# Optimization experiments

Hardware: AMD Instinct MI355X
Metric: run time of the kernel (lower is better)

## Reference

```python
import jax, jax.numpy as jnp
import numpy as np

H = 4      # n_heads
HD = 32    # head_dim
D = 128    # pair channels = H*HD
S = 384    # sequence length
EPS = 1e-5


def setup_inputs() -> dict:
    key = jax.random.key(0)
    ks = jax.random.split(key, 8)
    return {
        "x": jax.random.normal(ks[0], (1, S, S, D), dtype=jnp.float32),
        "attn_mask": jnp.zeros((1, 1, 1, S), dtype=jnp.float32),
        "ln_w": jax.random.uniform(ks[1], (D,), dtype=jnp.float32),
        "ln_b": jax.random.normal(ks[2], (D,), dtype=jnp.float32) * 0.02,
        "bias_w": jax.random.normal(ks[3], (H, D), dtype=jnp.float32) * 0.02,
        "qkv_w": jax.random.normal(ks[4], (3 * H * HD, D), dtype=jnp.float32) * 0.02,
        "g_w": jax.random.normal(ks[5], (H * HD, D), dtype=jnp.float32) * 0.02,
        "o_w": jax.random.normal(ks[6], (D, H * HD), dtype=jnp.float32) * 0.02,
    }


def reference(x, attn_mask, ln_w, ln_b, bias_w, qkv_w, g_w, o_w):
    # x: [1, S, S, D]; ending=False -> no permute
    xs = x[0]  # [S, S, D]; first S = batch of rows, second S = attended axis
    mu = jnp.mean(xs, axis=-1, keepdims=True)
    var = jnp.mean(jnp.square(xs - mu), axis=-1, keepdims=True)
    ln = (xs - mu) * jax.lax.rsqrt(var + EPS) * ln_w + ln_b  # [S, S, D]

    # triangle bias: D -> H, shaped [1, H, S, S], broadcast over row-batch
    bias = jnp.einsum('ijd,hd->hij', ln, bias_w)  # [H, S, S]

    # fused qkv projection, split heads
    qkv = jnp.einsum('bsd,ed->bse', ln, qkv_w)  # [S, S, 3*H*HD]
    q, k, v = jnp.split(qkv, 3, axis=-1)
    def heads(t):
        return t.reshape(S, S, H, HD).transpose(0, 2, 1, 3)  # [S, H, S, HD]
    q, k, v = heads(q), heads(k), heads(v)

    scale = 1.0 / jnp.sqrt(jnp.float32(HD))
    scores = jnp.einsum('bhqd,bhkd->bhqk', q, k) * scale  # [S, H, S, S]
    scores = scores + bias[None] + attn_mask  # attn_mask broadcasts [1,1,1,S]
    attn = jax.nn.softmax(scores, axis=-1)
    o = jnp.einsum('bhqk,bhkd->bhqd', attn, v)  # [S, H, S, HD]
    o = o.transpose(0, 2, 1, 3).reshape(S, S, H * HD)  # concat heads

    g = jnp.einsum('bsd,ed->bse', ln, g_w)  # [S, S, H*HD]
    o = o * jax.nn.sigmoid(g)
    out = jnp.einsum('bse,de->bsd', o, o_w)  # [S, S, D]
    return out[None]  # [1, S, S, D]
```

## Files before the change

### kernel.cpp

```cpp
#include <hip/hip_runtime.h>
#include <hip/hip_bf16.h>


#define S_ 384
#define D_ 128
#define MTOT (S_*S_)

typedef __bf16 bf16;
typedef __bf16 bf16x8 __attribute__((ext_vector_type(8)));
typedef __bf16 bf16x4 __attribute__((ext_vector_type(4)));
typedef float  f32x4  __attribute__((ext_vector_type(4)));

#define LOG2E      1.4426950408889634f
#define QSCALE     0.17677669529663687f
#define QSCALE_L2E 0.25505008455121566f

#if defined(__has_builtin)
#  if __has_builtin(__builtin_amdgcn_exp2f)
#    define HAVE_EXP2 1
#  else
#    define HAVE_EXP2 0
#  endif
#else
#  define HAVE_EXP2 0
#endif

#if HAVE_EXP2
#  define BIAS_MUL LOG2E
#  define Q_MUL    QSCALE_L2E
__device__ __forceinline__ float fast_pexp(float x) { return __builtin_amdgcn_exp2f(x); }
#else
#  define BIAS_MUL 1.0f
#  define Q_MUL    QSCALE
__device__ __forceinline__ float fast_pexp(float x) { return __expf(x); }
#endif

#define OFF_LN   0u
#define OFF_Q    37748736u
#define OFF_K    75497472u
#define OFF_V    113246208u
#define OFF_G    150994944u
#define OFF_BIAS 188743680u
#define OFF_W2   191102976u
#define OFF_OWB  191234048u

__global__ __launch_bounds__(256) void k0_convert(const float* __restrict__ qkv_w,
                                                  const float* __restrict__ g_w,
                                                  const float* __restrict__ o_w,
                                                  bf16* __restrict__ W2,
                                                  bf16* __restrict__ o_wb) {
    int idx = blockIdx.x * 256 + threadIdx.x;
    if (idx < 512 * 128) {
        float v = (idx < 384 * 128) ? qkv_w[idx] : g_w[idx - 384 * 128];
        W2[idx] = (bf16)v;
    }
    int idx2 = idx - 512 * 128;
    if (idx2 >= 0 && idx2 < 128 * 128) o_wb[idx2] = (bf16)o_w[idx2];
}

__global__ __launch_bounds__(256) void k1_ln(const float* __restrict__ x,
                                             const float* __restrict__ ln_w,
                                             const float* __restrict__ ln_b,
                                             const float* __restrict__ bias_w,
                                             const float* __restrict__ mask,
                                             bf16* __restrict__ ln_ws,
                                             float* __restrict__ bias_f) {
    int wid = threadIdx.x >> 6, lane = threadIdx.x & 63;
    int grp = lane >> 5, sub = lane & 31;
    int pos = blockIdx.x * 8 + wid * 2 + grp;
    f32x4 v = ((const f32x4*)(x + (size_t)pos * D_))[sub];
    float sum = v[0] + v[1] + v[2] + v[3];
    float ssq = v[0]*v[0] + v[1]*v[1] + v[2]*v[2] + v[3]*v[3];
    #pragma unroll
    for (int off = 16; off; off >>= 1) {
        sum += __shfl_xor(sum, off);
        ssq += __shfl_xor(ssq, off);
    }
    float mu   = sum * (1.0f / D_);
    float var  = ssq * (1.0f / D_) - mu * mu;
    float rstd = rsqrtf(var + 1e-5f);
    f32x4 w4 = ((const f32x4*)ln_w)[sub];
    f32x4 b4 = ((const f32x4*)ln_b)[sub];
    f32x4 y;
    #pragma unroll
    for (int i = 0; i < 4; ++i) y[i] = (v[i] - mu) * rstd * w4[i] + b4[i];
    bf16x4 yb;
    #pragma unroll
    for (int i = 0; i < 4; ++i) yb[i] = (bf16)y[i];
    *(bf16x4*)(ln_ws + (size_t)pos * D_ + 4 * sub) = yb;

    int ii = pos / S_, jj = pos - ii * S_;
    float mk = mask[jj];
    float p[4];
    #pragma unroll
    for (int h = 0; h < 4; ++h) {
        f32x4 bw = ((const f32x4*)(bias_w + h * D_))[sub];
        p[h] = y[0]*bw[0] + y[1]*bw[1] + y[2]*bw[2] + y[3]*bw[3];
    }
    #pragma unroll
    for (int off = 16; off; off >>= 1)
        #pragma unroll
        for (int h = 0; h < 4; ++h) p[h] += __shfl_xor(p[h], off);
    if (sub == 0) {
        int base = ((ii >> 4) * 24 + (jj >> 4)) * 256 + (((jj >> 2) & 3) * 16 + (ii & 15)) * 4 + (jj & 3);
        #pragma unroll
        for (int h = 0; h < 4; ++h)
            bias_f[h * 147456 + base] = (p[h] + mk) * BIAS_MUL;
    }
}

__global__ __launch_bounds__(256) void k2_proj(const bf16* __restrict__ ln_ws,
                                               const bf16* __restrict__ W2,
                                               bf16* __restrict__ q_ws,
                                               bf16* __restrict__ k_ws,
                                               bf16* __restrict__ v_ws,
                                               bf16* __restrict__ g_ws) {
    __shared__ __align__(16) char smem[64 * 272 + 128 * 272];
    char* As = smem;
    char* Bs = smem + 64 * 272;
    char* Cs = smem;
    int t = threadIdx.x;
    int bid = blockIdx.x;
    int by = bid & 3;
    int bx = bid >> 2;
    int m0 = bx * 64;
    int n0 = by * 128;
    #pragma unroll
    for (int it = 0; it < 4; ++it) {
        int byte = it * 4096 + t * 16;
        int row = byte >> 8, colb = byte & 255;
        *(int4*)(As + row * 272 + colb) = *(const int4*)((const char*)ln_ws + (size_t)(m0 + row) * 256 + colb);
    }
    #pragma unroll
    for (int it = 0; it < 8; ++it) {
        int byte = it * 4096 + t * 16;
        int row = byte >> 8, colb = byte & 255;
        *(int4*)(Bs + row * 272 + colb) = *(const int4*)((const char*)W2 + (size_t)(n0 + row) * 256 + colb);
    }
    __syncthreads();
    int wid = t >> 6, lane = t & 63, lr = lane & 15, g = lane >> 4;
    int wm = wid >> 1, wn = wid & 1;
    f32x4 acc[2][4] = {};
    #pragma unroll
    for (int ks = 0; ks < 4; ++ks) {
        bf16x8 af[2], bfr[4];
        #pragma unroll
        for (int mt = 0; mt < 2; ++mt)
            af[mt] = *(const bf16x8*)(As + (wm * 32 + mt * 16 + lr) * 272 + ks * 64 + g * 16);
        #pragma unroll
        for (int nt = 0; nt < 4; ++nt)
            bfr[nt] = *(const bf16x8*)(Bs + (wn * 64 + nt * 16 + lr) * 272 + ks * 64 + g * 16);
        #pragma unroll
        for (int mt = 0; mt < 2; ++mt)
            #pragma unroll
            for (int nt = 0; nt < 4; ++nt)
                acc[mt][nt] = __builtin_amdgcn_mfma_f32_16x16x32_bf16(af[mt], bfr[nt], acc[mt][nt], 0, 0, 0);
    }
    __syncthreads();
    float cmul = (by == 0) ? Q_MUL : 1.0f;
    #pragma unroll
    for (int mt = 0; mt < 2; ++mt)
        #pragma unroll
        for (int nt = 0; nt < 4; ++nt)
            #pragma unroll
            for (int i = 0; i < 4; ++i) {
                int ml = wm * 32 + mt * 16 + g * 4 + i;
                int nl = wn * 64 + nt * 16 + lr;
                *(bf16*)(Cs + ml * 272 + nl * 2) = (bf16)(acc[mt][nt][i] * cmul);
            }
    __syncthreads();
    int b = m0 / 384;
    int jj0 = m0 - b * 384;
    if (by < 2) {
        bf16* dst0 = (by == 0) ? q_ws : k_ws;
        size_t bh = (size_t)b * 4 + wid;
        bf16* dst = dst0 + bh * 12288 + (size_t)(jj0 >> 4) * 512 + lane * 8;
        #pragma unroll
        for (int tl = 0; tl < 4; ++tl) {
            bf16x8 v8 = *(const bf16x8*)(Cs + (tl * 16 + lr) * 272 + (wid * 32 + 8 * g) * 2);
            *(bf16x8*)(dst + tl * 512) = v8;
        }
    } else if (by == 2) {
        size_t bh = (size_t)b * 4 + wid;
        bf16* dst = v_ws + bh * 12288 + (size_t)(jj0 >> 5) * 1024 + lane * 8;
        #pragma unroll
        for (int f = 0; f < 4; ++f) {
            int kt64 = f >> 1, dt = f & 1;
            bf16x8 v8;
            #pragma unroll
            for (int j = 0; j < 8; ++j) {
                int kl = 16 * (j >> 2) + 4 * g + (j & 3);
                v8[j] = *(const bf16*)(Cs + (kt64 * 32 + kl) * 272 + (wid * 32 + dt * 16 + lr) * 2);
            }
            *(bf16x8*)(dst + kt64 * 1024 + dt * 512) = v8;
        }
    } else {
        #pragma unroll
        for (int j = 0; j < 4; ++j) {
            int byte = t * 64 + j * 16;
            int ml = byte >> 8, col = byte & 255;
            *(int4*)((char*)g_ws + (size_t)(m0 + ml) * 256 + col) = *(const int4*)(Cs + ml * 272 + col);
        }
    }
}

__global__ __launch_bounds__(512, 6) void k3_attn(const bf16* __restrict__ q_ws,
                                                  const bf16* __restrict__ k_ws,
                                                  const bf16* __restrict__ v_ws,
                                                  const float* __restrict__ bias_f,
                                                  bf16* __restrict__ o_ws) {
    __shared__ __align__(16) char smem[49152];
    char* Ksh = smem;
    char* Vsh = smem + 24576;
    int t = threadIdx.x;
    int bh = blockIdx.x;
    int b = bh >> 2, h = bh & 3;
    const char* kbase = (const char*)(k_ws + (size_t)bh * 12288);
    const char* vbase = (const char*)(v_ws + (size_t)bh * 12288);
    #pragma unroll
    for (int it = 0; it < 3; ++it) {
        int byte = it * 8192 + t * 16;
        *(int4*)(Ksh + byte) = *(const int4*)(kbase + byte);
        *(int4*)(Vsh + byte) = *(const int4*)(vbase + byte);
    }
    __syncthreads();
    int wid = t >> 6, lane = t & 63, lr = lane & 15, g = lane >> 4;
    const char* qbase = (const char*)(q_ws + (size_t)bh * 12288);
    const float* bbase = bias_f + (size_t)h * 147456;
    #pragma unroll 1
    for (int ch = 0; ch < 3; ++ch) {
        int qtile = ch * 8 + wid;
        bf16x8 qf = *(const bf16x8*)(qbase + qtile * 1024 + lane * 16);
        const f32x4* bptr = (const f32x4*)(bbase + qtile * 6144) + lane;
        f32x4 oa[2] = {};
        f32x4 lv = {};
        #pragma unroll 2
        for (int kt = 0; kt < 4; ++kt) {
            bf16x8 pf[3];
            #pragma unroll
            for (int nt = 0; nt < 6; ++nt) {
                int ktile = kt * 6 + nt;
                f32x4 b4 = bptr[ktile * 64];
                bf16x8 kf = *(const bf16x8*)(Ksh + ktile * 1024 + lane * 16);
                f32x4 acc = __builtin_amdgcn_mfma_f32_16x16x32_bf16(kf, qf, b4, 0, 0, 0);
                #pragma unroll
                for (int i = 0; i < 4; ++i) {
                    float p = fast_pexp(acc[i]);
                    lv[i] += p;
                    pf[nt >> 1][(nt & 1) * 4 + i] = (bf16)p;
                }
            }
            #pragma unroll
            for (int tt = 0; tt < 3; ++tt)
                #pragma unroll
                for (int dt = 0; dt < 2; ++dt) {
                    bf16x8 vf = *(const bf16x8*)(Vsh + (kt * 3 + tt) * 2048 + dt * 1024 + lane * 16);
                    oa[dt] = __builtin_amdgcn_mfma_f32_16x16x32_bf16(pf[tt], vf, oa[dt], 0, 0, 0);
                }
        }
        float l = lv[0] + lv[1] + lv[2] + lv[3];
        l += __shfl_xor(l, 16);
        l += __shfl_xor(l, 32);
        float inv = 1.0f / l;
        float invq[4];
        #pragma unroll
        for (int i = 0; i < 4; ++i) invq[i] = __shfl(inv, 4 * g + i);
        int q0 = qtile * 16;
        #pragma unroll
        for (int dt = 0; dt < 2; ++dt)
            #pragma unroll
            for (int i = 0; i < 4; ++i)
                o_ws[((size_t)b * 384 + q0 + 4 * g + i) * 128 + h * 32 + dt * 16 + lr] = (bf16)(oa[dt][i] * invq[i]);
    }
}

__global__ __launch_bounds__(256) void k4_out(const bf16* __restrict__ o_ws,
                                              const bf16* __restrict__ g_ws,
                                              const bf16* __restrict__ o_wb,
                                              float* __restrict__ out) {
    __shared__ __align__(16) char smem[64 * 272 + 128 * 272];
    char* As = smem;
    char* Bs = smem + 64 * 272;
    int t = threadIdx.x;
    int m0 = blockIdx.x * 64;
    #pragma unroll
    for (int it = 0; it < 4; ++it) {
        int byte = it * 4096 + t * 16;
        int row = byte >> 8, colb = byte & 255;
        bf16x8 o8 = *(const bf16x8*)((const char*)o_ws + (size_t)(m0 + row) * 256 + colb);
        bf16x8 g8 = *(const bf16x8*)((const char*)g_ws + (size_t)(m0 + row) * 256 + colb);
        bf16x8 a8;
        #pragma unroll
        for (int j = 0; j < 8; ++j) {
            float ov = (float)o8[j], gv = (float)g8[j];
            a8[j] = (bf16)(ov / (1.0f + __expf(-gv)));
        }
        *(bf16x8*)(As + row * 272 + colb) = a8;
    }
    #pragma unroll
    for (int it = 0; it < 8; ++it) {
        int byte = it * 4096 + t * 16;
        int row = byte >> 8, colb = byte & 255;
        *(int4*)(Bs + row * 272 + colb) = *(const int4*)((const char*)o_wb + (size_t)row * 256 + colb);
    }
    __syncthreads();
    int wid = t >> 6, lane = t & 63, lr = lane & 15, g = lane >> 4;
    int wm = wid >> 1, wn = wid & 1;
    f32x4 acc[2][4] = {};
    #pragma unroll
    for (int ks = 0; ks < 4; ++ks) {
        bf16x8 af[2], bfr[4];
        #pragma unroll
        for (int mt = 0; mt < 2; ++mt)
            af[mt] = *(const bf16x8*)(As + (wm * 32 + mt * 16 + lr) * 272 + ks * 64 + g * 16);
        #pragma unroll
        for (int nt = 0; nt < 4; ++nt)
            bfr[nt] = *(const bf16x8*)(Bs + (wn * 64 + nt * 16 + lr) * 272 + ks * 64 + g * 16);
        #pragma unroll
        for (int mt = 0; mt < 2; ++mt)
            #pragma unroll
            for (int nt = 0; nt < 4; ++nt)
                acc[mt][nt] = __builtin_amdgcn_mfma_f32_16x16x32_bf16(af[mt], bfr[nt], acc[mt][nt], 0, 0, 0);
    }
    #pragma unroll
    for (int mt = 0; mt < 2; ++mt)
        #pragma unroll
        for (int nt = 0; nt < 4; ++nt)
            #pragma unroll
            for (int i = 0; i < 4; ++i) {
                int m = m0 + wm * 32 + mt * 16 + g * 4 + i;
                int n = wn * 64 + nt * 16 + lr;
                out[(size_t)m * 128 + n] = acc[mt][nt][i];
            }
}

extern "C" void kernel_launch(void* const* d_in, const int* in_sizes, int n_in,
                              void* d_out, int out_size, void* d_ws, size_t ws_size,
                              hipStream_t stream) {
    const float* x      = (const float*)d_in[0];
    const float* mask   = (const float*)d_in[1];
    const float* ln_w   = (const float*)d_in[2];
    const float* ln_b   = (const float*)d_in[3];
    const float* bias_w = (const float*)d_in[4];
    const float* qkv_w  = (const float*)d_in[5];
    const float* g_w    = (const float*)d_in[6];
    const float* o_w    = (const float*)d_in[7];
    char* ws = (char*)d_ws;
    bf16*  ln_ws  = (bf16*)(ws + OFF_LN);
    bf16*  q_ws   = (bf16*)(ws + OFF_Q);
    bf16*  k_ws   = (bf16*)(ws + OFF_K);
    bf16*  v_ws   = (bf16*)(ws + OFF_V);
    bf16*  g_ws   = (bf16*)(ws + OFF_G);
    float* bias_f = (float*)(ws + OFF_BIAS);
    bf16*  W2     = (bf16*)(ws + OFF_W2);
    bf16*  o_wb   = (bf16*)(ws + OFF_OWB);
    bf16*  o_ws   = ln_ws;
    float* out    = (float*)d_out;

    k0_convert<<<dim3(320), dim3(256), 0, stream>>>(qkv_w, g_w, o_w, W2, o_wb);
    k1_ln<<<dim3(MTOT / 8), dim3(256), 0, stream>>>(x, ln_w, ln_b, bias_w, mask, ln_ws, bias_f);
    k2_proj<<<dim3(MTOT / 64 * 4), dim3(256), 0, stream>>>(ln_ws, W2, q_ws, k_ws, v_ws, g_ws);
    k3_attn<<<dim3(S_ * 4), dim3(512), 0, stream>>>(q_ws, k_ws, v_ws, bias_f, o_ws);
    k4_out<<<dim3(MTOT / 64), dim3(256), 0, stream>>>(o_ws, g_ws, o_wb, out);
}
```

Before: 196.2 us.

## Fuse LayerNorm and bias computation into the QKV/gate projection kernel

Merges the LayerNorm/bias kernel and the projection GEMM into one kernel. Each block normalizes 64 rows straight into shared memory and then loops over the four 128-column weight slices (Q, K, V, G). This removes the round trip of the bf16 LN activations through global memory and one kernel launch. In exchange, each block does four times the work serially and grid parallelism drops fourfold, with extra syncthreads between slices.

```diff
diff --git a/kernel.cpp b/kernel.cpp
--- a/kernel.cpp
+++ b/kernel.cpp
@@ -35,7 +35,7 @@
 __device__ __forceinline__ float fast_pexp(float x) { return __expf(x); }
 #endif
 
-#define OFF_LN   0u
+#define OFF_O    0u
 #define OFF_Q    37748736u
 #define OFF_K    75497472u
 #define OFF_V    113246208u
@@ -58,149 +58,151 @@
     if (idx2 >= 0 && idx2 < 128 * 128) o_wb[idx2] = (bf16)o_w[idx2];
 }
 
-__global__ __launch_bounds__(256) void k1_ln(const float* __restrict__ x,
-                                             const float* __restrict__ ln_w,
-                                             const float* __restrict__ ln_b,
-                                             const float* __restrict__ bias_w,
-                                             const float* __restrict__ mask,
-                                             bf16* __restrict__ ln_ws,
-                                             float* __restrict__ bias_f) {
-    int wid = threadIdx.x >> 6, lane = threadIdx.x & 63;
-    int grp = lane >> 5, sub = lane & 31;
-    int pos = blockIdx.x * 8 + wid * 2 + grp;
-    f32x4 v = ((const f32x4*)(x + (size_t)pos * D_))[sub];
-    float sum = v[0] + v[1] + v[2] + v[3];
-    float ssq = v[0]*v[0] + v[1]*v[1] + v[2]*v[2] + v[3]*v[3];
-    #pragma unroll
-    for (int off = 16; off; off >>= 1) {
-        sum += __shfl_xor(sum, off);
-        ssq += __shfl_xor(ssq, off);
-    }
+__global__ __launch_bounds__(256) void k12_lnproj(const float* __restrict__ x,
+                                                  const float* __restrict__ ln_w,
+                                                  const float* __restrict__ ln_b,
+                                                  const float* __restrict__ bias_w,
+                                                  const float* __restrict__ mask,
+                                                  const bf16* __restrict__ W2,
+                                                  bf16* __restrict__ q_ws,
+                                                  bf16* __restrict__ k_ws,
+                                                  bf16* __restrict__ v_ws,
+                                                  bf16* __restrict__ g_ws,
+                                                  float* __restrict__ bias_f) {
+    __shared__ __align__(16) char smem[17408 + 34816];
+    char* As = smem;
+    char* Bs = smem + 17408;
+    char* Cs = Bs;
+    int t = threadIdx.x;
+    int wid = t >> 6, lane = t & 63;
+    int m0 = blockIdx.x * 64;
+    int b = m0 / 384, jj0 = m0 - b * 384;
+
+    int r = (wid << 4) + (lane >> 2);
+    int q = lane & 3;
+    const float* xrow = x + (size_t)(m0 + r) * 128 + q * 32;
+    f32x4 xv[8];
+    #pragma unroll
+    for (int i = 0; i < 8; ++i) xv[i] = *(const f32x4*)(xrow + i * 4);
+    float sum = 0.f, ssq = 0.f;
+    #pragma unroll
+    for (int i = 0; i < 8; ++i)
+        #pragma unroll
+        for (int c = 0; c < 4; ++c) { float v = xv[i][c]; sum += v; ssq += v * v; }
+    sum += __shfl_xor(sum, 1); sum += __shfl_xor(sum, 2);
+    ssq += __shfl_xor(ssq, 1); ssq += __shfl_xor(ssq, 2);
     float mu   = sum * (1.0f / D_);
-    float var  = ssq * (1.0f / D_) - mu * mu;
-    float rstd = rsqrtf(var + 1e-5f);
-    f32x4 w4 = ((const f32x4*)ln_w)[sub];
-    f32x4 b4 = ((const f32x4*)ln_b)[sub];
-    f32x4 y;
-    #pragma unroll
-    for (int i = 0; i < 4; ++i) y[i] = (v[i] - mu) * rstd * w4[i] + b4[i];
-    bf16x4 yb;
-    #pragma unroll
-    for (int i = 0; i < 4; ++i) yb[i] = (bf16)y[i];
-    *(bf16x4*)(ln_ws + (size_t)pos * D_ + 4 * sub) = yb;
-
-    int ii = pos / S_, jj = pos - ii * S_;
-    float mk = mask[jj];
-    float p[4];
+    float rstd = rsqrtf(ssq * (1.0f / D_) - mu * mu + 1e-5f);
+    float y[32];
+    #pragma unroll
+    for (int i = 0; i < 8; ++i) {
+        f32x4 w4 = *(const f32x4*)(ln_w + q * 32 + i * 4);
+        f32x4 b4 = *(const f32x4*)(ln_b + q * 32 + i * 4);
+        #pragma unroll
+        for (int c = 0; c < 4; ++c)
+            y[i * 4 + c] = (xv[i][c] - mu) * rstd * w4[c] + b4[c];
+    }
+    #pragma unroll
+    for (int i2 = 0; i2 < 4; ++i2) {
+        bf16x8 v8;
+        #pragma unroll
+        for (int c = 0; c < 8; ++c) v8[c] = (bf16)y[i2 * 8 + c];
+        *(bf16x8*)(As + r * 272 + q * 64 + i2 * 16) = v8;
+    }
+    float pd[4];
     #pragma unroll
     for (int h = 0; h < 4; ++h) {
-        f32x4 bw = ((const f32x4*)(bias_w + h * D_))[sub];
-        p[h] = y[0]*bw[0] + y[1]*bw[1] + y[2]*bw[2] + y[3]*bw[3];
-    }
-    #pragma unroll
-    for (int off = 16; off; off >>= 1)
-        #pragma unroll
-        for (int h = 0; h < 4; ++h) p[h] += __shfl_xor(p[h], off);
-    if (sub == 0) {
-        int base = ((ii >> 4) * 24 + (jj >> 4)) * 256 + (((jj >> 2) & 3) * 16 + (ii & 15)) * 4 + (jj & 3);
-        #pragma unroll
-        for (int h = 0; h < 4; ++h)
-            bias_f[h * 147456 + base] = (p[h] + mk) * BIAS_MUL;
-    }
-}
-
-__global__ __launch_bounds__(256) void k2_proj(const bf16* __restrict__ ln_ws,
-                                               const bf16* __restrict__ W2,
-                                               bf16* __restrict__ q_ws,
-                                               bf16* __restrict__ k_ws,
-                                               bf16* __restrict__ v_ws,
-                                               bf16* __restrict__ g_ws) {
-    __shared__ __align__(16) char smem[64 * 272 + 128 * 272];
-    char* As = smem;
-    char* Bs = smem + 64 * 272;
-    char* Cs = smem;
-    int t = threadIdx.x;
-    int bid = blockIdx.x;
-    int by = bid & 3;
-    int bx = bid >> 2;
-    int m0 = bx * 64;
-    int n0 = by * 128;
-    #pragma unroll
-    for (int it = 0; it < 4; ++it) {
-        int byte = it * 4096 + t * 16;
-        int row = byte >> 8, colb = byte & 255;
-        *(int4*)(As + row * 272 + colb) = *(const int4*)((const char*)ln_ws + (size_t)(m0 + row) * 256 + colb);
-    }
-    #pragma unroll
-    for (int it = 0; it < 8; ++it) {
-        int byte = it * 4096 + t * 16;
-        int row = byte >> 8, colb = byte & 255;
-        *(int4*)(Bs + row * 272 + colb) = *(const int4*)((const char*)W2 + (size_t)(n0 + row) * 256 + colb);
+        float s = 0.f;
+        #pragma unroll
+        for (int i = 0; i < 8; ++i) {
+            f32x4 bw = *(const f32x4*)(bias_w + h * 128 + q * 32 + i * 4);
+            #pragma unroll
+            for (int c = 0; c < 4; ++c) s += y[i * 4 + c] * bw[c];
+        }
+        pd[h] = s;
+    }
+    #pragma unroll
+    for (int h = 0; h < 4; ++h) { pd[h] += __shfl_xor(pd[h], 1); pd[h] += __shfl_xor(pd[h], 2); }
+    {
+        int jj = jj0 + r;
+        int base = ((b >> 4) * 24 + (jj >> 4)) * 256 + (((jj >> 2) & 3) * 16 + (b & 15)) * 4 + (jj & 3);
+        bias_f[q * 147456 + base] = (pd[q] + mask[jj]) * BIAS_MUL;
     }
     __syncthreads();
-    int wid = t >> 6, lane = t & 63, lr = lane & 15, g = lane >> 4;
+
+    int lr = lane & 15, g = lane >> 4;
     int wm = wid >> 1, wn = wid & 1;
-    f32x4 acc[2][4] = {};
-    #pragma unroll
-    for (int ks = 0; ks < 4; ++ks) {
-        bf16x8 af[2], bfr[4];
+    #pragma unroll 1
+    for (int by = 0; by < 4; ++by) {
+        int n0 = by * 128;
+        #pragma unroll
+        for (int it = 0; it < 8; ++it) {
+            int byte = it * 4096 + t * 16;
+            int row = byte >> 8, colb = byte & 255;
+            *(int4*)(Bs + row * 272 + colb) = *(const int4*)((const char*)W2 + (size_t)(n0 + row) * 256 + colb);
+        }
+        __syncthreads();
+        f32x4 acc[2][4] = {};
+        #pragma unroll
+        for (int ks = 0; ks < 4; ++ks) {
+            bf16x8 af[2], bfr[4];
+            #pragma unroll
+            for (int mt = 0; mt < 2; ++mt)
+                af[mt] = *(const bf16x8*)(As + (wm * 32 + mt * 16 + lr) * 272 + ks * 64 + g * 16);
+            #pragma unroll
+            for (int nt = 0; nt < 4; ++nt)
+                bfr[nt] = *(const bf16x8*)(Bs + (wn * 64 + nt * 16 + lr) * 272 + ks * 64 + g * 16);
+            #pragma unroll
+            for (int mt = 0; mt < 2; ++mt)
+                #pragma unroll
+                for (int nt = 0; nt < 4; ++nt)
+                    acc[mt][nt] = __builtin_amdgcn_mfma_f32_16x16x32_bf16(af[mt], bfr[nt], acc[mt][nt], 0, 0, 0);
+        }
+        __syncthreads();
+        float cmul = (by == 0) ? Q_MUL : 1.0f;
         #pragma unroll
         for (int mt = 0; mt < 2; ++mt)
-            af[mt] = *(const bf16x8*)(As + (wm * 32 + mt * 16 + lr) * 272 + ks * 64 + g * 16);
-        #pragma unroll
-        for (int nt = 0; nt < 4; ++nt)
-            bfr[nt] = *(const bf16x8*)(Bs + (wn * 64 + nt * 16 + lr) * 272 + ks * 64 + g * 16);
-        #pragma unroll
-        for (int mt = 0; mt < 2; ++mt)
             #pragma unroll
             for (int nt = 0; nt < 4; ++nt)
-                acc[mt][nt] = __builtin_amdgcn_mfma_f32_16x16x32_bf16(af[mt], bfr[nt], acc[mt][nt], 0, 0, 0);
-    }
-    __syncthreads();
-    float cmul = (by == 0) ? Q_MUL : 1.0f;
-    #pragma unroll
-    for (int mt = 0; mt < 2; ++mt)
-        #pragma unroll
-        for (int nt = 0; nt < 4; ++nt)
-            #pragma unroll
-            for (int i = 0; i < 4; ++i) {
-                int ml = wm * 32 + mt * 16 + g * 4 + i;
-                int nl = wn * 64 + nt * 16 + lr;
-                *(bf16*)(Cs + ml * 272 + nl * 2) = (bf16)(acc[mt][nt][i] * cmul);
-            }
-    __syncthreads();
-    int b = m0 / 384;
-    int jj0 = m0 - b * 384;
-    if (by < 2) {
-        bf16* dst0 = (by == 0) ? q_ws : k_ws;
-        size_t bh = (size_t)b * 4 + wid;
-        bf16* dst = dst0 + bh * 12288 + (size_t)(jj0 >> 4) * 512 + lane * 8;
-        #pragma unroll
-        for (int tl = 0; tl < 4; ++tl) {
-            bf16x8 v8 = *(const bf16x8*)(Cs + (tl * 16 + lr) * 272 + (wid * 32 + 8 * g) * 2);
-            *(bf16x8*)(dst + tl * 512) = v8;
-        }
-    } else if (by == 2) {
-        size_t bh = (size_t)b * 4 + wid;
-        bf16* dst = v_ws + bh * 12288 + (size_t)(jj0 >> 5) * 1024 + lane * 8;
-        #pragma unroll
-        for (int f = 0; f < 4; ++f) {
-            int kt64 = f >> 1, dt = f & 1;
-            bf16x8 v8;
-            #pragma unroll
-            for (int j = 0; j < 8; ++j) {
-                int kl = 16 * (j >> 2) + 4 * g + (j & 3);
-                v8[j] = *(const bf16*)(Cs + (kt64 * 32 + kl) * 272 + (wid * 32 + dt * 16 + lr) * 2);
-            }
-            *(bf16x8*)(dst + kt64 * 1024 + dt * 512) = v8;
-        }
-    } else {
-        #pragma unroll
-        for (int j = 0; j < 4; ++j) {
-            int byte = t * 64 + j * 16;
-            int ml = byte >> 8, col = byte & 255;
-            *(int4*)((char*)g_ws + (size_t)(m0 + ml) * 256 + col) = *(const int4*)(Cs + ml * 272 + col);
-        }
+                #pragma unroll
+                for (int i = 0; i < 4; ++i) {
+                    int ml = wm * 32 + mt * 16 + g * 4 + i;
+                    int nl = wn * 64 + nt * 16 + lr;
+                    *(bf16*)(Cs + ml * 272 + nl * 2) = (bf16)(acc[mt][nt][i] * cmul);
+                }
+        __syncthreads();
+        if (by < 2) {
+            bf16* dst0 = (by == 0) ? q_ws : k_ws;
+            size_t bh = (size_t)b * 4 + wid;
+            bf16* dst = dst0 + bh * 12288 + (size_t)(jj0 >> 4) * 512 + lane * 8;
+            #pragma unroll
+            for (int tl = 0; tl < 4; ++tl) {
+                bf16x8 v8 = *(const bf16x8*)(Cs + (tl * 16 + lr) * 272 + (wid * 32 + 8 * g) * 2);
+                *(bf16x8*)(dst + tl * 512) = v8;
+            }
+        } else if (by == 2) {
+            size_t bh = (size_t)b * 4 + wid;
+            bf16* dst = v_ws + bh * 12288 + (size_t)(jj0 >> 5) * 1024 + lane * 8;
+            #pragma unroll
+            for (int f = 0; f < 4; ++f) {
+                int kt64 = f >> 1, dt = f & 1;
+                bf16x8 v8;
+                #pragma unroll
+                for (int j = 0; j < 8; ++j) {
+                    int kl = 16 * (j >> 2) + 4 * g + (j & 3);
+                    v8[j] = *(const bf16*)(Cs + (kt64 * 32 + kl) * 272 + (wid * 32 + dt * 16 + lr) * 2);
+                }
+                *(bf16x8*)(dst + kt64 * 1024 + dt * 512) = v8;
+            }
+        } else {
+            #pragma unroll
+            for (int j = 0; j < 4; ++j) {
+                int byte = t * 64 + j * 16;
+                int ml = byte >> 8, col = byte & 255;
+                *(int4*)((char*)g_ws + (size_t)(m0 + ml) * 256 + col) = *(const int4*)(Cs + ml * 272 + col);
+            }
+        }
+        __syncthreads();
     }
 }
 
@@ -346,7 +348,7 @@
     const float* g_w    = (const float*)d_in[6];
     const float* o_w    = (const float*)d_in[7];
     char* ws = (char*)d_ws;
-    bf16*  ln_ws  = (bf16*)(ws + OFF_LN);
+    bf16*  o_ws   = (bf16*)(ws + OFF_O);
     bf16*  q_ws   = (bf16*)(ws + OFF_Q);
     bf16*  k_ws   = (bf16*)(ws + OFF_K);
     bf16*  v_ws   = (bf16*)(ws + OFF_V);
@@ -354,12 +356,11 @@
     float* bias_f = (float*)(ws + OFF_BIAS);
     bf16*  W2     = (bf16*)(ws + OFF_W2);
     bf16*  o_wb   = (bf16*)(ws + OFF_OWB);
-    bf16*  o_ws   = ln_ws;
     float* out    = (float*)d_out;
 
     k0_convert<<<dim3(320), dim3(256), 0, stream>>>(qkv_w, g_w, o_w, W2, o_wb);
-    k1_ln<<<dim3(MTOT / 8), dim3(256), 0, stream>>>(x, ln_w, ln_b, bias_w, mask, ln_ws, bias_f);
-    k2_proj<<<dim3(MTOT / 64 * 4), dim3(256), 0, stream>>>(ln_ws, W2, q_ws, k_ws, v_ws, g_ws);
+    k12_lnproj<<<dim3(MTOT / 64), dim3(256), 0, stream>>>(x, ln_w, ln_b, bias_w, mask, W2,
+                                                          q_ws, k_ws, v_ws, g_ws, bias_f);
     k3_attn<<<dim3(S_ * 4), dim3(512), 0, stream>>>(q_ws, k_ws, v_ws, bias_f, o_ws);
     k4_out<<<dim3(MTOT / 64), dim3(256), 0, stream>>>(o_ws, g_ws, o_wb, out);
 }
```

Result: slower. 203.5 us (+3.7%).
